# Performance work log

Hardware: AMD Instinct MI355X
Metric: run time of the kernel (lower is better)

## Reference

```python
import jax, jax.numpy as jnp
import numpy as np

N_ATOMS = 50000
ATOM_FDIM = 133
HIDDEN = 128
DEPTH = 3
N_EDGES = 800000
N_MOLS = 1024
BN_EPS = 1e-5


def setup_inputs() -> dict:
    key = jax.random.key(0)
    ks = jax.random.split(key, 10)
    f_atoms = jax.random.normal(ks[0], (N_ATOMS, ATOM_FDIM), dtype=jnp.float32)
    W_in = jax.random.normal(ks[1], (ATOM_FDIM, HIDDEN), dtype=jnp.float32) / np.sqrt(ATOM_FDIM)
    b_in = jax.random.normal(ks[2], (HIDDEN,), dtype=jnp.float32) * 0.01
    W1 = jax.random.normal(ks[3], (DEPTH, HIDDEN, HIDDEN), dtype=jnp.float32) / np.sqrt(HIDDEN)
    b1 = jax.random.normal(ks[4], (DEPTH, HIDDEN), dtype=jnp.float32) * 0.01
    W2 = jax.random.normal(ks[5], (DEPTH, HIDDEN, HIDDEN), dtype=jnp.float32) / np.sqrt(HIDDEN)
    b2 = jax.random.normal(ks[6], (DEPTH, HIDDEN), dtype=jnp.float32) * 0.01
    gamma = jnp.ones((DEPTH, HIDDEN), dtype=jnp.float32)
    beta = jnp.zeros((DEPTH, HIDDEN), dtype=jnp.float32)
    eps_param = jnp.zeros((DEPTH,), dtype=jnp.float32)
    edge_index = jax.random.randint(ks[7], (2, N_EDGES), 0, N_ATOMS, dtype=jnp.int64 if jax.config.jax_enable_x64 else jnp.int32).astype(jnp.int32)
    segment_ids = jnp.sort(jax.random.randint(ks[8], (N_ATOMS,), 0, N_MOLS).astype(jnp.int32))
    return {"f_atoms": f_atoms, "W_in": W_in, "b_in": b_in, "W1": W1, "b1": b1,
            "W2": W2, "b2": b2, "gamma": gamma, "beta": beta, "eps_param": eps_param,
            "edge_index": edge_index, "segment_ids": segment_ids}


def _gin_forward(f_atoms, W_in, b_in, W1, b1, W2, b2, gamma, beta, eps_param,
                 edge_index, segment_ids):
    src, tgt = edge_index[0], edge_index[1]
    # input projection + ReLU
    x = jax.nn.relu(f_atoms @ W_in + b_in)  # [N, H]
    for d in range(DEPTH):
        # scatter-add of gathered neighbor features + (1+eps) self term
        agg = jnp.zeros_like(x).at[tgt].add(x[src]) + (1.0 + eps_param[d]) * x
        h = jax.nn.relu(agg @ W1[d] + b1[d])
        h = h @ W2[d] + b2[d]
        # BatchNorm1d (training-mode batch statistics)
        mean = jnp.mean(h, axis=0)
        var = jnp.var(h, axis=0)
        h = gamma[d] * (h - mean) * jax.lax.rsqrt(var + BN_EPS) + beta[d]
        x = jax.nn.relu(h)
    # per-molecule mean pooling (a_scope -> segment mean); empty mols -> zeros
    sums = jax.ops.segment_sum(x, segment_ids, num_segments=N_MOLS)  # [M, H]
    counts = jax.ops.segment_sum(jnp.ones((x.shape[0],), x.dtype), segment_ids,
                                 num_segments=N_MOLS)
    mol_vecs = jnp.where(counts[:, None] > 0, sums / jnp.maximum(counts, 1.0)[:, None], 0.0)
    return mol_vecs


def reference(f_atoms, W_in, b_in, W1, b1, W2, b2, gamma, beta, eps_param,
              edge_index, segment_ids):
    return _gin_forward(f_atoms, W_in, b_in, W1, b1, W2, b2, gamma, beta,
                        eps_param, edge_index, segment_ids)
```

## Files before the change

### kernel.cpp

```cpp
#include <hip/hip_runtime.h>
#include <hip/hip_fp16.h>

#define N_ATOMS   50000
#define ATOM_FDIM 133
#define HIDDEN    128
#define DEPTH     3
#define N_EDGES   800000
#define N_MOLS    1024
#define BN_EPS    1e-5f
#define K_IN_PAD  160

typedef _Float16 f16x8 __attribute__((ext_vector_type(8)));
typedef _Float16 f16x2 __attribute__((ext_vector_type(2)));
typedef float    f32x4 __attribute__((ext_vector_type(4)));

struct __align__(8) half4pack { __half2 a, b; };

__global__ void hist_kernel(const int* __restrict__ idx, int n, int* __restrict__ cnt) {
    int i = blockIdx.x * blockDim.x + threadIdx.x;
    if (i < n) atomicAdd(&cnt[idx[i]], 1);
}

__global__ void scan_block_kernel(const int* __restrict__ in, int* __restrict__ out,
                                  int* __restrict__ bsum, int n) {
    __shared__ int buf[256];
    int i = blockIdx.x * 256 + threadIdx.x;
    int v = (i < n) ? in[i] : 0;
    buf[threadIdx.x] = v;
    __syncthreads();
    #pragma unroll
    for (int off = 1; off < 256; off <<= 1) {
        int t = (threadIdx.x >= off) ? buf[threadIdx.x - off] : 0;
        __syncthreads();
        buf[threadIdx.x] += t;
        __syncthreads();
    }
    if (i < n) out[i] = buf[threadIdx.x] - v;
    if (threadIdx.x == 255) bsum[blockIdx.x] = buf[255];
}

__global__ void scan_top_kernel(int* __restrict__ bsum, int nb) {
    __shared__ int buf[256];
    int v = (threadIdx.x < nb) ? bsum[threadIdx.x] : 0;
    buf[threadIdx.x] = v;
    __syncthreads();
    #pragma unroll
    for (int off = 1; off < 256; off <<= 1) {
        int t = (threadIdx.x >= off) ? buf[threadIdx.x - off] : 0;
        __syncthreads();
        buf[threadIdx.x] += t;
        __syncthreads();
    }
    if (threadIdx.x < nb) bsum[threadIdx.x] = buf[threadIdx.x] - v;
}

__global__ void scan_add_kernel(const int* __restrict__ partial, const int* __restrict__ bsum,
                                int* __restrict__ rowptr, int* __restrict__ wcur,
                                int n, int total) {
    int i = blockIdx.x * 256 + threadIdx.x;
    if (i < n) {
        int v = partial[i] + bsum[blockIdx.x];
        rowptr[i] = v;
        wcur[i]   = v;
    }
    if (i == 0) rowptr[n] = total;
}

#define FB (N_EDGES / 256)
__global__ void fill_setup_kernel(const int* __restrict__ src, const int* __restrict__ tgt,
                                  int* __restrict__ wcur, unsigned short* __restrict__ col,
                                  const float* __restrict__ f,
                                  const float* __restrict__ W_in,
                                  const float* __restrict__ W1,
                                  const float* __restrict__ W2,
                                  const int* __restrict__ seg,
                                  __half* __restrict__ Ah, __half* __restrict__ Wt,
                                  float* __restrict__ stats, int* __restrict__ moloff)
{
    if (blockIdx.x < FB) {
        int e = blockIdx.x * 256 + threadIdx.x;
        int t = tgt[e];
        int p = atomicAdd(&wcur[t], 1);
        col[p] = (unsigned short)src[e];
        return;
    }
    const int NCH = N_ATOMS * (K_IN_PAD / 4);
    const int NW4 = (128 * K_IN_PAD + 2 * DEPTH * 128 * 128) / 4;
    int i = (blockIdx.x - FB) * 256 + threadIdx.x;
    if (i < NCH) {
        int row = i / (K_IN_PAD / 4);
        int c4  = (i - row * (K_IN_PAD / 4)) * 4;
        float v[4];
        #pragma unroll
        for (int u = 0; u < 4; ++u) {
            int k = c4 + u;
            v[u] = (k < ATOM_FDIM) ? f[(size_t)row * ATOM_FDIM + k] : 0.f;
        }
        half4pack p;
        p.a = __float22half2_rn(make_float2(v[0], v[1]));
        p.b = __float22half2_rn(make_float2(v[2], v[3]));
        *(half4pack*)&Ah[(size_t)row * K_IN_PAD + c4] = p;
        return;
    }
    int j = i - NCH;
    if (j < NW4) {
        float v[4];
        #pragma unroll
        for (int u = 0; u < 4; ++u) {
            int e = j * 4 + u;
            if (e < 128 * K_IN_PAD) {
                int n = e / K_IN_PAD, k = e - n * K_IN_PAD;
                v[u] = (k < ATOM_FDIM) ? W_in[(size_t)k * 128 + n] : 0.f;
            } else if (e < 128 * K_IN_PAD + DEPTH * 128 * 128) {
                int q = e - 128 * K_IN_PAD;
                int d = q >> 14, r = q & 16383;
                int n = r >> 7, k = r & 127;
                v[u] = W1[((size_t)d * 128 + k) * 128 + n];
            } else {
                int q = e - 128 * K_IN_PAD - DEPTH * 128 * 128;
                int d = q >> 14, r = q & 16383;
                int n = r >> 7, k = r & 127;
                v[u] = W2[((size_t)d * 128 + k) * 128 + n];
            }
        }
        half4pack p;
        p.a = __float22half2_rn(make_float2(v[0], v[1]));
        p.b = __float22half2_rn(make_float2(v[2], v[3]));
        *(half4pack*)&Wt[j * 4] = p;
        return;
    }
    int m = j - NW4;
    if (m < DEPTH * 256) stats[m] = 0.f;
    if (m <= N_MOLS) {
        int lo = 0, hi = N_ATOMS;
        while (lo < hi) {
            int mid = (lo + hi) >> 1;
            if (seg[mid] < m) lo = mid + 1; else hi = mid;
        }
        moloff[m] = lo;
    }
}

#define LDS_S 40

template<bool RELU>
__global__ __launch_bounds__(256, 2) void mfma_gemm(
    const __half* __restrict__ A, const __half* __restrict__ Bt,
    const float* __restrict__ bias, __half* __restrict__ C, int M, int K)
{
    __shared__ __align__(16) __half As[128 * LDS_S];
    __shared__ __align__(16) __half Bs[128 * LDS_S];

    const int t = threadIdx.x;
    const int w = t >> 6, lane = t & 63;
    const int wm = w >> 1, wn = w & 1;
    const int l15 = lane & 15, quad = lane >> 4;
    const int row0 = blockIdx.x * 128;

    f32x4 acc[4][4];
    #pragma unroll
    for (int mt = 0; mt < 4; ++mt)
        #pragma unroll
        for (int nt = 0; nt < 4; ++nt) acc[mt][nt] = (f32x4){0.f, 0.f, 0.f, 0.f};

    for (int k0 = 0; k0 < K; k0 += 32) {
        #pragma unroll
        for (int i = 0; i < 2; ++i) {
            int c = t * 2 + i;
            int r = c >> 2, o = c & 3;
            int row = row0 + r;
            uint4 v = make_uint4(0, 0, 0, 0);
            if (row < M) v = *(const uint4*)&A[(size_t)row * K + k0 + o * 8];
            *(uint4*)&As[r * LDS_S + o * 8] = v;
        }
        #pragma unroll
        for (int i = 0; i < 2; ++i) {
            int c = t * 2 + i;
            int r = c >> 2, o = c & 3;
            uint4 v = *(const uint4*)&Bt[(size_t)r * K + k0 + o * 8];
            *(uint4*)&Bs[r * LDS_S + o * 8] = v;
        }
        __syncthreads();
        f16x8 af[4], bf[4];
        #pragma unroll
        for (int mt = 0; mt < 4; ++mt)
            af[mt] = *(const f16x8*)&As[(wm * 64 + mt * 16 + l15) * LDS_S + quad * 8];
        #pragma unroll
        for (int nt = 0; nt < 4; ++nt)
            bf[nt] = *(const f16x8*)&Bs[(wn * 64 + nt * 16 + l15) * LDS_S + quad * 8];
        #pragma unroll
        for (int mt = 0; mt < 4; ++mt)
            #pragma unroll
            for (int nt = 0; nt < 4; ++nt)
                acc[mt][nt] = __builtin_amdgcn_mfma_f32_16x16x32_f16(af[mt], bf[nt], acc[mt][nt], 0, 0, 0);
        __syncthreads();
    }

    #pragma unroll
    for (int nt = 0; nt < 4; ++nt) {
        int col = wn * 64 + nt * 16 + l15;
        float b = bias[col];
        #pragma unroll
        for (int mt = 0; mt < 4; ++mt) {
            #pragma unroll
            for (int r = 0; r < 4; ++r) {
                int row = row0 + wm * 64 + mt * 16 + quad * 4 + r;
                if (row < M) {
                    float o = acc[mt][nt][r] + b;
                    if (RELU) o = fmaxf(o, 0.f);
                    C[(size_t)row * 128 + col] = __float2half(o);
                }
            }
        }
    }
}

__global__ __launch_bounds__(256, 2) void mlp_fused(
    const __half* __restrict__ A, const __half* __restrict__ B1t,
    const __half* __restrict__ B2t,
    const float* __restrict__ bias1, const float* __restrict__ bias2,
    __half* __restrict__ C, int M,
    float* __restrict__ s1, float* __restrict__ s2)
{
    __shared__ __align__(16) __half As[4 * 128 * LDS_S];
    __shared__ __align__(16) __half Bs[4 * 128 * LDS_S];

    const int t = threadIdx.x;
    const int w = t >> 6, lane = t & 63;
    const int wm = w >> 1, wn = w & 1;
    const int l15 = lane & 15, quad = lane >> 4;
    const int row0 = blockIdx.x * 128;

    f32x4 acc[4][4];
    #pragma unroll
    for (int mt = 0; mt < 4; ++mt)
        #pragma unroll
        for (int nt = 0; nt < 4; ++nt) acc[mt][nt] = (f32x4){0.f, 0.f, 0.f, 0.f};

    #pragma unroll
    for (int i = 0; i < 8; ++i) {
        int c = i * 256 + t;
        int r = c >> 4, o = c & 15;
        int kc = o >> 2, oo = o & 3;
        int row = row0 + r;
        uint4 v = make_uint4(0, 0, 0, 0);
        if (row < M) v = *(const uint4*)&A[(size_t)row * 128 + o * 8];
        *(uint4*)&As[(kc * 128 + r) * LDS_S + oo * 8] = v;
    }
    #pragma unroll
    for (int i = 0; i < 8; ++i) {
        int c = i * 256 + t;
        int r = c >> 4, o = c & 15;
        int kc = o >> 2, oo = o & 3;
        uint4 v = *(const uint4*)&B1t[(size_t)r * 128 + o * 8];
        *(uint4*)&Bs[(kc * 128 + r) * LDS_S + oo * 8] = v;
    }
    __syncthreads();

    #pragma unroll
    for (int kc = 0; kc < 4; ++kc) {
        f16x8 af[4], bf[4];
        #pragma unroll
        for (int mt = 0; mt < 4; ++mt)
            af[mt] = *(const f16x8*)&As[(kc * 128 + wm * 64 + mt * 16 + l15) * LDS_S + quad * 8];
        #pragma unroll
        for (int nt = 0; nt < 4; ++nt)
            bf[nt] = *(const f16x8*)&Bs[(kc * 128 + wn * 64 + nt * 16 + l15) * LDS_S + quad * 8];
        #pragma unroll
        for (int mt = 0; mt < 4; ++mt)
            #pragma unroll
            for (int nt = 0; nt < 4; ++nt)
                acc[mt][nt] = __builtin_amdgcn_mfma_f32_16x16x32_f16(af[mt], bf[nt], acc[mt][nt], 0, 0, 0);
    }
    __syncthreads();

    #pragma unroll
    for (int nt = 0; nt < 4; ++nt) {
        int k = wn * 64 + nt * 16 + l15;
        float b = bias1[k];
        int kc = k >> 5, ko = k & 31;
        #pragma unroll
        for (int mt = 0; mt < 4; ++mt) {
            #pragma unroll
            for (int r = 0; r < 4; ++r) {
                int rl = wm * 64 + mt * 16 + quad * 4 + r;
                float h = fmaxf(acc[mt][nt][r] + b, 0.f);
                As[(kc * 128 + rl) * LDS_S + ko] = __float2half(h);
            }
        }
    }
    #pragma unroll
    for (int i = 0; i < 8; ++i) {
        int c = i * 256 + t;
        int r = c >> 4, o = c & 15;
        int kc = o >> 2, oo = o & 3;
        uint4 v = *(const uint4*)&B2t[(size_t)r * 128 + o * 8];
        *(uint4*)&Bs[(kc * 128 + r) * LDS_S + oo * 8] = v;
    }
    __syncthreads();

    #pragma unroll
    for (int mt = 0; mt < 4; ++mt)
        #pragma unroll
        for (int nt = 0; nt < 4; ++nt) acc[mt][nt] = (f32x4){0.f, 0.f, 0.f, 0.f};
    #pragma unroll
    for (int kc = 0; kc < 4; ++kc) {
        f16x8 af[4], bf[4];
        #pragma unroll
        for (int mt = 0; mt < 4; ++mt)
            af[mt] = *(const f16x8*)&As[(kc * 128 + wm * 64 + mt * 16 + l15) * LDS_S + quad * 8];
        #pragma unroll
        for (int nt = 0; nt < 4; ++nt)
            bf[nt] = *(const f16x8*)&Bs[(kc * 128 + wn * 64 + nt * 16 + l15) * LDS_S + quad * 8];
        #pragma unroll
        for (int mt = 0; mt < 4; ++mt)
            #pragma unroll
            for (int nt = 0; nt < 4; ++nt)
                acc[mt][nt] = __builtin_amdgcn_mfma_f32_16x16x32_f16(af[mt], bf[nt], acc[mt][nt], 0, 0, 0);
    }

    float ps[4] = {0, 0, 0, 0}, pss[4] = {0, 0, 0, 0};
    #pragma unroll
    for (int nt = 0; nt < 4; ++nt) {
        int col = wn * 64 + nt * 16 + l15;
        float b = bias2[col];
        #pragma unroll
        for (int mt = 0; mt < 4; ++mt) {
            #pragma unroll
            for (int r = 0; r < 4; ++r) {
                int row = row0 + wm * 64 + mt * 16 + quad * 4 + r;
                if (row < M) {
                    float o = acc[mt][nt][r] + b;
                    ps[nt] += o;
                    pss[nt] += o * o;
                    C[(size_t)row * 128 + col] = __float2half(o);
                }
            }
        }
    }

    float* red1 = (float*)As;
    float* red2 = (float*)Bs;
    int contrib = wm * 4 + quad;
    __syncthreads();
    #pragma unroll
    for (int nt = 0; nt < 4; ++nt) {
        int col = wn * 64 + nt * 16 + l15;
        red1[contrib * 128 + col] = ps[nt];
        red2[contrib * 128 + col] = pss[nt];
    }
    __syncthreads();
    if (t < 128) {
        float s = 0.f, q = 0.f;
        #pragma unroll
        for (int g = 0; g < 8; ++g) {
            s += red1[g * 128 + t];
            q += red2[g * 128 + t];
        }
        atomicAdd(&s1[t], s);
        atomicAdd(&s2[t], q);
    }
}

template<bool BN>
__global__ __launch_bounds__(256) void aggregate_kernel(
    const f16x2* __restrict__ xh2, const int* __restrict__ rowptr,
    const unsigned short* __restrict__ col, const float* __restrict__ eps_param, int d,
    const float* __restrict__ s1, const float* __restrict__ s2,
    const float* __restrict__ gamma, const float* __restrict__ beta, int dprev,
    f16x2* __restrict__ aggh2)
{
    int gw = (blockIdx.x * 256 + threadIdx.x) >> 6;
    int lane = threadIdx.x & 63;
    float e1 = 1.0f + eps_param[d];

    float sc_x = 1.f, sc_y = 1.f, c_x = 0.f, c_y = 0.f;
    f16x2 c2 = (f16x2){(_Float16)0.f, (_Float16)0.f};
    if (BN) {
        const float inv_n = 1.0f / (float)N_ATOMS;
        int c0 = lane * 2;
        float m0 = s1[c0] * inv_n;
        float v0 = fmaxf(s2[c0] * inv_n - m0 * m0, 0.f);
        float m1 = s1[c0 + 1] * inv_n;
        float v1 = fmaxf(s2[c0 + 1] * inv_n - m1 * m1, 0.f);
        sc_x = gamma[dprev * 128 + c0]     * rsqrtf(v0 + BN_EPS);
        sc_y = gamma[dprev * 128 + c0 + 1] * rsqrtf(v1 + BN_EPS);
        c_x = beta[dprev * 128 + c0]     / sc_x - m0;
        c_y = beta[dprev * 128 + c0 + 1] / sc_y - m1;
        c2 = (f16x2){(_Float16)c_x, (_Float16)c_y};
    }

    f16x2 ah = xh2[(size_t)gw * 64 + lane];
    float2 a = make_float2((float)ah.x, (float)ah.y);
    if (BN) {
        a.x = sc_x * fmaxf(a.x + c_x, 0.f);
        a.y = sc_y * fmaxf(a.y + c_y, 0.f);
    }
    float2 acc;
    acc.x = a.x * e1;
    acc.y = a.y * e1;

    const f16x2 z2 = (f16x2){(_Float16)0.f, (_Float16)0.f};
    int s = rowptr[gw], e = rowptr[gw + 1];
    int i = s;
    for (; i + 8 <= e; i += 8) {
        f16x2 v[8];
        #pragma unroll
        for (int u = 0; u < 8; ++u) {
            int c = col[i + u];
            v[u] = xh2[(size_t)c * 64 + lane];
        }
        if (BN) {
            #pragma unroll
            for (int u = 0; u < 8; ++u)
                v[u] = __builtin_elementwise_max(v[u] + c2, z2);
        }
        f16x2 p0 = v[0] + v[1], p1 = v[2] + v[3];
        f16x2 p2 = v[4] + v[5], p3 = v[6] + v[7];
        f16x2 r2 = (p0 + p1) + (p2 + p3);
        float frx = (float)r2.x, fry = (float)r2.y;
        if (BN) {
            acc.x = fmaf(sc_x, frx, acc.x);
            acc.y = fmaf(sc_y, fry, acc.y);
        } else {
            acc.x += frx;
            acc.y += fry;
        }
    }
    if (i < e) {
        f16x2 v[8];
        #pragma unroll
        for (int u = 0; u < 8; ++u) {
            int idx = min(i + u, e - 1);
            int c = col[idx];
            v[u] = xh2[(size_t)c * 64 + lane];
        }
        #pragma unroll
        for (int u = 0; u < 8; ++u) {
            float fx = (float)v[u].x, fy = (float)v[u].y;
            if (BN) {
                fx = sc_x * fmaxf(fx + c_x, 0.f);
                fy = sc_y * fmaxf(fy + c_y, 0.f);
            }
            if (i + u < e) {
                acc.x += fx;
                acc.y += fy;
            }
        }
    }
    aggh2[(size_t)gw * 64 + lane] = (f16x2){(_Float16)acc.x, (_Float16)acc.y};
}

__global__ void pool_kernel(const __half* __restrict__ hh, const int* __restrict__ off,
                            const float* __restrict__ s1, const float* __restrict__ s2,
                            const float* __restrict__ gamma, const float* __restrict__ beta,
                            int dprev, float* __restrict__ out)
{
    int m = blockIdx.x;
    int c = threadIdx.x;
    const float inv_n = 1.0f / (float)N_ATOMS;
    float mean = s1[c] * inv_n;
    float var = fmaxf(s2[c] * inv_n - mean * mean, 0.f);
    float sc = gamma[dprev * 128 + c] * rsqrtf(var + BN_EPS);
    float sh = beta[dprev * 128 + c] - mean * sc;
    int s = off[m], e = off[m + 1];
    float acc = 0.f;
    for (int r = s; r < e; ++r) {
        float v = __half2float(hh[(size_t)r * 128 + c]);
        acc += fmaxf(v * sc + sh, 0.f);
    }
    int cnt = e - s;
    out[m * 128 + c] = (cnt > 0) ? acc / (float)cnt : 0.f;
}

extern "C" void kernel_launch(void* const* d_in, const int* in_sizes, int n_in,
                              void* d_out, int out_size, void* d_ws, size_t ws_size,
                              hipStream_t stream)
{
    const float* f_atoms   = (const float*)d_in[0];
    const float* W_in      = (const float*)d_in[1];
    const float* b_in      = (const float*)d_in[2];
    const float* W1        = (const float*)d_in[3];
    const float* b1        = (const float*)d_in[4];
    const float* W2        = (const float*)d_in[5];
    const float* b2        = (const float*)d_in[6];
    const float* gamma     = (const float*)d_in[7];
    const float* beta      = (const float*)d_in[8];
    const float* eps_param = (const float*)d_in[9];
    const int*   edge_index= (const int*)d_in[10];
    const int*   seg       = (const int*)d_in[11];
    const int*   src = edge_index;
    const int*   tgt = edge_index + N_EDGES;
    float* out = (float*)d_out;

    char* ws = (char*)d_ws;
    size_t off = 0;
    auto alloc = [&](size_t bytes) -> char* {
        char* p = ws + off;
        off += (bytes + 255) & ~(size_t)255;
        return p;
    };
    __half* xh    = (__half*)alloc((size_t)N_ATOMS * HIDDEN * 2);
    __half* aggh  = (__half*)alloc((size_t)N_ATOMS * HIDDEN * 2);
    __half* hpre  = (__half*)alloc((size_t)N_ATOMS * HIDDEN * 2);
    __half* Ah    = (__half*)alloc((size_t)N_ATOMS * K_IN_PAD * 2);
    __half* Wt    = (__half*)alloc((size_t)(128 * K_IN_PAD + 2 * DEPTH * 128 * 128) * 2);
    int*   rowptr = (int*)alloc((N_ATOMS + 1) * 4);
    int*   wcur   = (int*)alloc(N_ATOMS * 4);
    int*   partial= (int*)alloc(N_ATOMS * 4);
    int*   bsum   = (int*)alloc(256 * 4);
    unsigned short* col = (unsigned short*)alloc((size_t)N_EDGES * 2);
    float* s12    = (float*)alloc(DEPTH * 256 * 4);
    int*   moloff = (int*)alloc((N_MOLS + 1) * 4);

    const __half* Wt_in = Wt;
    const __half* W1t   = Wt + 128 * K_IN_PAD;
    const __half* W2t   = W1t + DEPTH * 128 * 128;

    hipMemsetAsync(wcur, 0, N_ATOMS * 4, stream);
    hist_kernel<<<(N_EDGES + 255) / 256, 256, 0, stream>>>(tgt, N_EDGES, wcur);
    const int NB = (N_ATOMS + 255) / 256;
    scan_block_kernel<<<NB, 256, 0, stream>>>(wcur, partial, bsum, N_ATOMS);
    scan_top_kernel<<<1, 256, 0, stream>>>(bsum, NB);
    scan_add_kernel<<<NB, 256, 0, stream>>>(partial, bsum, rowptr, wcur, N_ATOMS, N_EDGES);

    {
        const int NCH = N_ATOMS * (K_IN_PAD / 4);
        const int NW4 = (128 * K_IN_PAD + 2 * DEPTH * 128 * 128) / 4;
        const int SB  = (NCH + NW4 + N_MOLS + 1 + 255) / 256;
        fill_setup_kernel<<<FB + SB, 256, 0, stream>>>(
            src, tgt, wcur, col, f_atoms, W_in, W1, W2, seg, Ah, Wt, s12, moloff);
    }

    const int GB = (N_ATOMS + 127) / 128;
    mfma_gemm<true><<<GB, 256, 0, stream>>>(Ah, Wt_in, b_in, xh, N_ATOMS, K_IN_PAD);

    for (int d = 0; d < DEPTH; ++d) {
        float* s1d = s12 + d * 256;
        float* s2d = s1d + 128;
        if (d == 0) {
            aggregate_kernel<false><<<N_ATOMS / 4, 256, 0, stream>>>(
                (const f16x2*)xh, rowptr, col, eps_param, d,
                nullptr, nullptr, nullptr, nullptr, 0, (f16x2*)aggh);
        } else {
            float* s1p = s12 + (d - 1) * 256;
            float* s2p = s1p + 128;
            aggregate_kernel<true><<<N_ATOMS / 4, 256, 0, stream>>>(
                (const f16x2*)hpre, rowptr, col, eps_param, d,
                s1p, s2p, gamma, beta, d - 1, (f16x2*)aggh);
        }
        mlp_fused<<<GB, 256, 0, stream>>>(
            aggh, W1t + (size_t)d * 128 * 128, W2t + (size_t)d * 128 * 128,
            b1 + d * HIDDEN, b2 + d * HIDDEN, hpre, N_ATOMS, s1d, s2d);
    }

    pool_kernel<<<N_MOLS, 128, 0, stream>>>(
        hpre, moloff, s12 + (DEPTH - 1) * 256, s12 + (DEPTH - 1) * 256 + 128,
        gamma, beta, DEPTH - 1, out);
}
```

Baseline: 391.9 us.

## Split aggregation by channel groups, fuse scan top-level and CSR fill into GEMM

The preprocessing is restructured. The histogram is merged into the conversion kernel, the top-level scan is folded into scan_add as a per-block reduction, and the CSR fill runs inside the input-projection GEMM launch as extra blocks. The aggregation kernel now splits the 128 channels into 4 groups of 32 across separate blocks, with blocks interleaved so each feature slice stays cache-friendly. Within a group, 4 edge slots are spread across the lanes and combined with shuffle reductions. This adds more blocks and narrower per-lane loads in exchange for higher memory parallelism per atom and fewer launches.

```diff
diff --git a/kernel.cpp b/kernel.cpp
--- a/kernel.cpp
+++ b/kernel.cpp
@@ -16,77 +16,27 @@
 
 struct __align__(8) half4pack { __half2 a, b; };
 
-__global__ void hist_kernel(const int* __restrict__ idx, int n, int* __restrict__ cnt) {
-    int i = blockIdx.x * blockDim.x + threadIdx.x;
-    if (i < n) atomicAdd(&cnt[idx[i]], 1);
-}
-
-__global__ void scan_block_kernel(const int* __restrict__ in, int* __restrict__ out,
-                                  int* __restrict__ bsum, int n) {
-    __shared__ int buf[256];
-    int i = blockIdx.x * 256 + threadIdx.x;
-    int v = (i < n) ? in[i] : 0;
-    buf[threadIdx.x] = v;
-    __syncthreads();
-    #pragma unroll
-    for (int off = 1; off < 256; off <<= 1) {
-        int t = (threadIdx.x >= off) ? buf[threadIdx.x - off] : 0;
-        __syncthreads();
-        buf[threadIdx.x] += t;
-        __syncthreads();
-    }
-    if (i < n) out[i] = buf[threadIdx.x] - v;
-    if (threadIdx.x == 255) bsum[blockIdx.x] = buf[255];
-}
-
-__global__ void scan_top_kernel(int* __restrict__ bsum, int nb) {
-    __shared__ int buf[256];
-    int v = (threadIdx.x < nb) ? bsum[threadIdx.x] : 0;
-    buf[threadIdx.x] = v;
-    __syncthreads();
-    #pragma unroll
-    for (int off = 1; off < 256; off <<= 1) {
-        int t = (threadIdx.x >= off) ? buf[threadIdx.x - off] : 0;
-        __syncthreads();
-        buf[threadIdx.x] += t;
-        __syncthreads();
-    }
-    if (threadIdx.x < nb) bsum[threadIdx.x] = buf[threadIdx.x] - v;
-}
-
-__global__ void scan_add_kernel(const int* __restrict__ partial, const int* __restrict__ bsum,
-                                int* __restrict__ rowptr, int* __restrict__ wcur,
-                                int n, int total) {
-    int i = blockIdx.x * 256 + threadIdx.x;
-    if (i < n) {
-        int v = partial[i] + bsum[blockIdx.x];
-        rowptr[i] = v;
-        wcur[i]   = v;
-    }
-    if (i == 0) rowptr[n] = total;
-}
-
+#define HB (N_EDGES / 256)
 #define FB (N_EDGES / 256)
-__global__ void fill_setup_kernel(const int* __restrict__ src, const int* __restrict__ tgt,
-                                  int* __restrict__ wcur, unsigned short* __restrict__ col,
-                                  const float* __restrict__ f,
-                                  const float* __restrict__ W_in,
-                                  const float* __restrict__ W1,
-                                  const float* __restrict__ W2,
-                                  const int* __restrict__ seg,
-                                  __half* __restrict__ Ah, __half* __restrict__ Wt,
-                                  float* __restrict__ stats, int* __restrict__ moloff)
+#define GB_IN ((N_ATOMS + 127) / 128)
+
+__global__ void hist_conv_kernel(const int* __restrict__ tgt, int* __restrict__ cnt,
+                                 const float* __restrict__ f,
+                                 const float* __restrict__ W_in,
+                                 const float* __restrict__ W1,
+                                 const float* __restrict__ W2,
+                                 const int* __restrict__ seg,
+                                 __half* __restrict__ Ah, __half* __restrict__ Wt,
+                                 float* __restrict__ stats, int* __restrict__ moloff)
 {
-    if (blockIdx.x < FB) {
-        int e = blockIdx.x * 256 + threadIdx.x;
-        int t = tgt[e];
-        int p = atomicAdd(&wcur[t], 1);
-        col[p] = (unsigned short)src[e];
+    if (blockIdx.x < HB) {
+        int i = blockIdx.x * 256 + threadIdx.x;
+        atomicAdd(&cnt[tgt[i]], 1);
         return;
     }
     const int NCH = N_ATOMS * (K_IN_PAD / 4);
     const int NW4 = (128 * K_IN_PAD + 2 * DEPTH * 128 * 128) / 4;
-    int i = (blockIdx.x - FB) * 256 + threadIdx.x;
+    int i = (blockIdx.x - HB) * 256 + threadIdx.x;
     if (i < NCH) {
         int row = i / (K_IN_PAD / 4);
         int c4  = (i - row * (K_IN_PAD / 4)) * 4;
@@ -141,15 +91,64 @@
     }
 }
 
+__global__ void scan_block_kernel(const int* __restrict__ in, int* __restrict__ out,
+                                  int* __restrict__ bsum, int n) {
+    __shared__ int buf[256];
+    int i = blockIdx.x * 256 + threadIdx.x;
+    int v = (i < n) ? in[i] : 0;
+    buf[threadIdx.x] = v;
+    __syncthreads();
+    #pragma unroll
+    for (int off = 1; off < 256; off <<= 1) {
+        int t = (threadIdx.x >= off) ? buf[threadIdx.x - off] : 0;
+        __syncthreads();
+        buf[threadIdx.x] += t;
+        __syncthreads();
+    }
+    if (i < n) out[i] = buf[threadIdx.x] - v;
+    if (threadIdx.x == 255) bsum[blockIdx.x] = buf[255];
+}
+
+__global__ void scan_add2_kernel(const int* __restrict__ partial, const int* __restrict__ bsum,
+                                 int* __restrict__ rowptr, int* __restrict__ wcur,
+                                 int n, int total) {
+    __shared__ int red[256];
+    int v = ((int)threadIdx.x < (int)blockIdx.x) ? bsum[threadIdx.x] : 0;
+    red[threadIdx.x] = v;
+    __syncthreads();
+    #pragma unroll
+    for (int o = 128; o > 0; o >>= 1) {
+        if (threadIdx.x < o) red[threadIdx.x] += red[threadIdx.x + o];
+        __syncthreads();
+    }
+    int base = red[0];
+    int i = blockIdx.x * 256 + threadIdx.x;
+    if (i < n) {
+        int val = partial[i] + base;
+        rowptr[i] = val;
+        wcur[i]   = val;
+    }
+    if (i == 0) rowptr[n] = total;
+}
+
 #define LDS_S 40
 
-template<bool RELU>
-__global__ __launch_bounds__(256, 2) void mfma_gemm(
+__global__ __launch_bounds__(256, 2) void gemm_fill_kernel(
     const __half* __restrict__ A, const __half* __restrict__ Bt,
-    const float* __restrict__ bias, __half* __restrict__ C, int M, int K)
+    const float* __restrict__ bias, __half* __restrict__ C, int M, int K,
+    const int* __restrict__ src, const int* __restrict__ tgt,
+    int* __restrict__ wcur, unsigned short* __restrict__ col)
 {
     __shared__ __align__(16) __half As[128 * LDS_S];
     __shared__ __align__(16) __half Bs[128 * LDS_S];
+
+    if (blockIdx.x >= GB_IN) {
+        int e = (blockIdx.x - GB_IN) * 256 + threadIdx.x;
+        int t = tgt[e];
+        int p = atomicAdd(&wcur[t], 1);
+        col[p] = (unsigned short)src[e];
+        return;
+    }
 
     const int t = threadIdx.x;
     const int w = t >> 6, lane = t & 63;
@@ -198,17 +197,16 @@
 
     #pragma unroll
     for (int nt = 0; nt < 4; ++nt) {
-        int col = wn * 64 + nt * 16 + l15;
-        float b = bias[col];
+        int colc = wn * 64 + nt * 16 + l15;
+        float b = bias[colc];
         #pragma unroll
         for (int mt = 0; mt < 4; ++mt) {
             #pragma unroll
             for (int r = 0; r < 4; ++r) {
                 int row = row0 + wm * 64 + mt * 16 + quad * 4 + r;
                 if (row < M) {
-                    float o = acc[mt][nt][r] + b;
-                    if (RELU) o = fmaxf(o, 0.f);
-                    C[(size_t)row * 128 + col] = __float2half(o);
+                    float o = fmaxf(acc[mt][nt][r] + b, 0.f);
+                    C[(size_t)row * 128 + colc] = __float2half(o);
                 }
             }
         }
@@ -363,22 +361,28 @@
 }
 
 template<bool BN>
-__global__ __launch_bounds__(256) void aggregate_kernel(
+__global__ __launch_bounds__(256) void aggregate_cs_kernel(
     const f16x2* __restrict__ xh2, const int* __restrict__ rowptr,
     const unsigned short* __restrict__ col, const float* __restrict__ eps_param, int d,
     const float* __restrict__ s1, const float* __restrict__ s2,
     const float* __restrict__ gamma, const float* __restrict__ beta, int dprev,
     f16x2* __restrict__ aggh2)
 {
-    int gw = (blockIdx.x * 256 + threadIdx.x) >> 6;
-    int lane = threadIdx.x & 63;
-    float e1 = 1.0f + eps_param[d];
+    const int b = blockIdx.x;
+    const int g = (b & 7) >> 1;
+    const int idx = (b >> 3) * 2 + (b & 1);
+    const int wv = threadIdx.x >> 6;
+    const int atom = idx * 4 + wv;
+    const int lane = threadIdx.x & 63;
+    const int es = lane >> 4;
+    const int cp = lane & 15;
+    const int cpg = g * 16 + cp;
+    const float e1 = 1.0f + eps_param[d];
 
     float sc_x = 1.f, sc_y = 1.f, c_x = 0.f, c_y = 0.f;
-    f16x2 c2 = (f16x2){(_Float16)0.f, (_Float16)0.f};
     if (BN) {
         const float inv_n = 1.0f / (float)N_ATOMS;
-        int c0 = lane * 2;
+        int c0 = cpg * 2;
         float m0 = s1[c0] * inv_n;
         float v0 = fmaxf(s2[c0] * inv_n - m0 * m0, 0.f);
         float m1 = s1[c0 + 1] * inv_n;
@@ -387,68 +391,57 @@
         sc_y = gamma[dprev * 128 + c0 + 1] * rsqrtf(v1 + BN_EPS);
         c_x = beta[dprev * 128 + c0]     / sc_x - m0;
         c_y = beta[dprev * 128 + c0 + 1] / sc_y - m1;
-        c2 = (f16x2){(_Float16)c_x, (_Float16)c_y};
-    }
-
-    f16x2 ah = xh2[(size_t)gw * 64 + lane];
-    float2 a = make_float2((float)ah.x, (float)ah.y);
-    if (BN) {
-        a.x = sc_x * fmaxf(a.x + c_x, 0.f);
-        a.y = sc_y * fmaxf(a.y + c_y, 0.f);
-    }
-    float2 acc;
-    acc.x = a.x * e1;
-    acc.y = a.y * e1;
-
-    const f16x2 z2 = (f16x2){(_Float16)0.f, (_Float16)0.f};
-    int s = rowptr[gw], e = rowptr[gw + 1];
+    }
+
+    float2 acc = make_float2(0.f, 0.f);
+    const int s = rowptr[atom], e = rowptr[atom + 1];
     int i = s;
     for (; i + 8 <= e; i += 8) {
-        f16x2 v[8];
-        #pragma unroll
-        for (int u = 0; u < 8; ++u) {
-            int c = col[i + u];
-            v[u] = xh2[(size_t)c * 64 + lane];
-        }
+        int ca = col[i + es];
+        int cb = col[i + 4 + es];
+        f16x2 va = xh2[(size_t)ca * 64 + cpg];
+        f16x2 vb = xh2[(size_t)cb * 64 + cpg];
+        float ax = (float)va.x, ay = (float)va.y;
+        float bx = (float)vb.x, by = (float)vb.y;
         if (BN) {
-            #pragma unroll
-            for (int u = 0; u < 8; ++u)
-                v[u] = __builtin_elementwise_max(v[u] + c2, z2);
-        }
-        f16x2 p0 = v[0] + v[1], p1 = v[2] + v[3];
-        f16x2 p2 = v[4] + v[5], p3 = v[6] + v[7];
-        f16x2 r2 = (p0 + p1) + (p2 + p3);
-        float frx = (float)r2.x, fry = (float)r2.y;
+            ax = sc_x * fmaxf(ax + c_x, 0.f);
+            ay = sc_y * fmaxf(ay + c_y, 0.f);
+            bx = sc_x * fmaxf(bx + c_x, 0.f);
+            by = sc_y * fmaxf(by + c_y, 0.f);
+        }
+        acc.x += ax + bx;
+        acc.y += ay + by;
+    }
+    for (; i < e; i += 4) {
+        int idx2 = i + es;
+        int c = col[min(idx2, e - 1)];
+        f16x2 v = xh2[(size_t)c * 64 + cpg];
+        float fx = (float)v.x, fy = (float)v.y;
         if (BN) {
-            acc.x = fmaf(sc_x, frx, acc.x);
-            acc.y = fmaf(sc_y, fry, acc.y);
-        } else {
-            acc.x += frx;
-            acc.y += fry;
-        }
-    }
-    if (i < e) {
-        f16x2 v[8];
-        #pragma unroll
-        for (int u = 0; u < 8; ++u) {
-            int idx = min(i + u, e - 1);
-            int c = col[idx];
-            v[u] = xh2[(size_t)c * 64 + lane];
-        }
-        #pragma unroll
-        for (int u = 0; u < 8; ++u) {
-            float fx = (float)v[u].x, fy = (float)v[u].y;
-            if (BN) {
-                fx = sc_x * fmaxf(fx + c_x, 0.f);
-                fy = sc_y * fmaxf(fy + c_y, 0.f);
-            }
-            if (i + u < e) {
-                acc.x += fx;
-                acc.y += fy;
-            }
-        }
-    }
-    aggh2[(size_t)gw * 64 + lane] = (f16x2){(_Float16)acc.x, (_Float16)acc.y};
+            fx = sc_x * fmaxf(fx + c_x, 0.f);
+            fy = sc_y * fmaxf(fy + c_y, 0.f);
+        }
+        if (idx2 < e) {
+            acc.x += fx;
+            acc.y += fy;
+        }
+    }
+    acc.x += __shfl_xor(acc.x, 16, 64);
+    acc.y += __shfl_xor(acc.y, 16, 64);
+    acc.x += __shfl_xor(acc.x, 32, 64);
+    acc.y += __shfl_xor(acc.y, 32, 64);
+
+    if (es == 0) {
+        f16x2 ah = xh2[(size_t)atom * 64 + cpg];
+        float ax = (float)ah.x, ay = (float)ah.y;
+        if (BN) {
+            ax = sc_x * fmaxf(ax + c_x, 0.f);
+            ay = sc_y * fmaxf(ay + c_y, 0.f);
+        }
+        acc.x += ax * e1;
+        acc.y += ay * e1;
+        aggh2[(size_t)atom * 64 + cpg] = (f16x2){(_Float16)acc.x, (_Float16)acc.y};
+    }
 }
 
 __global__ void pool_kernel(const __half* __restrict__ hh, const int* __restrict__ off,
@@ -518,38 +511,36 @@
     const __half* W2t   = W1t + DEPTH * 128 * 128;
 
     hipMemsetAsync(wcur, 0, N_ATOMS * 4, stream);
-    hist_kernel<<<(N_EDGES + 255) / 256, 256, 0, stream>>>(tgt, N_EDGES, wcur);
-    const int NB = (N_ATOMS + 255) / 256;
-    scan_block_kernel<<<NB, 256, 0, stream>>>(wcur, partial, bsum, N_ATOMS);
-    scan_top_kernel<<<1, 256, 0, stream>>>(bsum, NB);
-    scan_add_kernel<<<NB, 256, 0, stream>>>(partial, bsum, rowptr, wcur, N_ATOMS, N_EDGES);
-
     {
         const int NCH = N_ATOMS * (K_IN_PAD / 4);
         const int NW4 = (128 * K_IN_PAD + 2 * DEPTH * 128 * 128) / 4;
-        const int SB  = (NCH + NW4 + N_MOLS + 1 + 255) / 256;
-        fill_setup_kernel<<<FB + SB, 256, 0, stream>>>(
-            src, tgt, wcur, col, f_atoms, W_in, W1, W2, seg, Ah, Wt, s12, moloff);
-    }
-
-    const int GB = (N_ATOMS + 127) / 128;
-    mfma_gemm<true><<<GB, 256, 0, stream>>>(Ah, Wt_in, b_in, xh, N_ATOMS, K_IN_PAD);
+        const int CB  = (NCH + NW4 + N_MOLS + 1 + 255) / 256;
+        hist_conv_kernel<<<HB + CB, 256, 0, stream>>>(
+            tgt, wcur, f_atoms, W_in, W1, W2, seg, Ah, Wt, s12, moloff);
+    }
+
+    const int NB = (N_ATOMS + 255) / 256;
+    scan_block_kernel<<<NB, 256, 0, stream>>>(wcur, partial, bsum, N_ATOMS);
+    scan_add2_kernel<<<NB, 256, 0, stream>>>(partial, bsum, rowptr, wcur, N_ATOMS, N_EDGES);
+
+    gemm_fill_kernel<<<GB_IN + FB, 256, 0, stream>>>(
+        Ah, Wt_in, b_in, xh, N_ATOMS, K_IN_PAD, src, tgt, wcur, col);
 
     for (int d = 0; d < DEPTH; ++d) {
         float* s1d = s12 + d * 256;
         float* s2d = s1d + 128;
         if (d == 0) {
-            aggregate_kernel<false><<<N_ATOMS / 4, 256, 0, stream>>>(
+            aggregate_cs_kernel<false><<<N_ATOMS, 256, 0, stream>>>(
                 (const f16x2*)xh, rowptr, col, eps_param, d,
                 nullptr, nullptr, nullptr, nullptr, 0, (f16x2*)aggh);
         } else {
             float* s1p = s12 + (d - 1) * 256;
             float* s2p = s1p + 128;
-            aggregate_kernel<true><<<N_ATOMS / 4, 256, 0, stream>>>(
+            aggregate_cs_kernel<true><<<N_ATOMS, 256, 0, stream>>>(
                 (const f16x2*)hpre, rowptr, col, eps_param, d,
                 s1p, s2p, gamma, beta, d - 1, (f16x2*)aggh);
         }
-        mlp_fused<<<GB, 256, 0, stream>>>(
+        mlp_fused<<<GB_IN, 256, 0, stream>>>(
             aggh, W1t + (size_t)d * 128 * 128, W2t + (size_t)d * 128 * 128,
             b1 + d * HIDDEN, b2 + d * HIDDEN, hpre, N_ATOMS, s1d, s2d);
     }
```

Measured after the change: 543.3 us. 38.6% more time.
